# Performance work log

Measured on AMD Instinct MI355X. Metric: run time of the kernel, lower is better.

Reference implementation:

```python
import jax, jax.numpy as jnp
import numpy as np

N = 200000      # total nodes
NG = 100000     # masked (graph) nodes
NU = N - NG     # unconnected nodes
E = 3200000     # edges (index into graph nodes)
C = 1000000     # candidate pairs


def setup_inputs() -> dict:
    key = jax.random.key(0)
    ks = jax.random.split(key, 16)
    s = 0.1  # weight init scale
    x = jax.random.normal(ks[0], (N, 2), jnp.float32)
    mask = jnp.arange(N) < NG
    candidates = jnp.stack([
        jax.random.randint(ks[1], (C,), 0, NG),
        jax.random.randint(ks[2], (C,), 0, NU),
    ], axis=1).astype(jnp.int32)
    edges = jax.random.randint(ks[3], (2, E), 0, NG).astype(jnp.int32)
    return {
        "x": x, "mask": mask, "candidates": candidates, "edges": edges,
        # GraphConv(2,8): lin_rel on aggregated neighbors, lin_root on self, bias in rel
        "w1_rel": jax.random.normal(ks[4], (2, 8), jnp.float32) * s,
        "w1_root": jax.random.normal(ks[5], (2, 8), jnp.float32) * s,
        "b1": jnp.zeros((8,), jnp.float32),
        # GraphConv(8,16)
        "w2_rel": jax.random.normal(ks[6], (8, 16), jnp.float32) * s,
        "w2_root": jax.random.normal(ks[7], (8, 16), jnp.float32) * s,
        "b2": jnp.zeros((16,), jnp.float32),
        # fc_unconnected: Linear(2,16) (source's Linear(8,16) is inconsistent with 2-dim x)
        "wu": jax.random.normal(ks[8], (2, 16), jnp.float32) * s,
        "bu": jnp.zeros((16,), jnp.float32),
        # fc: Linear(32,64) -> ReLU -> Linear(64,1)
        "wa": jax.random.normal(ks[9], (32, 64), jnp.float32) * s,
        "ba": jnp.zeros((64,), jnp.float32),
        "wb": jax.random.normal(ks[10], (64, 1), jnp.float32) * s,
        "bb": jnp.zeros((1,), jnp.float32),
    }


def graph_conv(h, edges, w_rel, w_root, b, n):
    # PyG GraphConv with aggr='add': out_i = W_rel @ sum_{j->i} h_j + W_root @ h_i + b
    src, dst = edges[0], edges[1]
    agg = jax.ops.segment_sum(h[src], dst, num_segments=n)  # [n, d_in]
    return agg @ w_rel + h @ w_root + b


def reference(x, mask, candidates, edges, w1_rel, w1_root, b1,
              w2_rel, w2_root, b2, wu, bu, wa, ba, wb, bb):
    idx_g = jnp.nonzero(mask, size=NG)[0]      # graph node indices
    idx_u = jnp.nonzero(~mask, size=NU)[0]     # unconnected node indices
    x_unconnected = x[idx_u] @ wu + bu                         # [NU, 16]
    h = jax.nn.relu(graph_conv(x[idx_g], edges, w1_rel, w1_root, b1, NG))  # [NG, 8]
    h = jax.nn.relu(graph_conv(h, edges, w2_rel, w2_root, b2, NG))         # [NG, 16]
    ec = jnp.concatenate([h[candidates[:, 0]], x_unconnected[candidates[:, 1]]], axis=-1)  # [C, 32]
    hid = jax.nn.relu(ec @ wa + ba)            # [C, 64]
    return jnp.squeeze(hid @ wb + bb, -1)      # [C]
```

## Files before the change

kernel.cpp:

```cpp
#include <hip/hip_runtime.h>

#define N_TOT  200000
#define NG_    100000
#define NU_    100000
#define E_CNT  3200000
#define C_CNT  1000000

#define NBUCK  196
#define NBLK   256
#define CHUNK  12500

#define CBLK   250
#define CCHUNK 4000
#define CCH_E  3907

#define DCAP   17920


__global__ __launch_bounds__(1024) void phaseA_f(const int* __restrict__ dst,
                                                 const int* __restrict__ cand,
                                                 int* __restrict__ cnt_mat,
                                                 int* __restrict__ cnt2) {
    __shared__ int hcnt[NBUCK];
    int t = threadIdx.x;
    if (t < NBUCK) hcnt[t] = 0;
    __syncthreads();
    int beg = blockIdx.x * CHUNK, end = beg + CHUNK;
    for (int e = beg + t; e < end; e += 1024)
        atomicAdd(&hcnt[dst[e] >> 9], 1);
    __syncthreads();
    if (t < NBUCK) { cnt_mat[blockIdx.x * NBUCK + t] = hcnt[t]; hcnt[t] = 0; }
    __syncthreads();
    int cbeg = blockIdx.x * CCH_E;
    int cend = min(cbeg + CCH_E, C_CNT);
    for (int e = cbeg + t; e < cend; e += 1024)
        atomicAdd(&hcnt[cand[2 * e] >> 9], 1);
    __syncthreads();
    if (t < NBUCK) cnt2[blockIdx.x * NBUCK + t] = hcnt[t];
}

__global__ __launch_bounds__(256) void phaseB1_f(const int* __restrict__ cnt_mat,
                                                 const int* __restrict__ cnt2,
                                                 int* __restrict__ off_mat,
                                                 int* __restrict__ off2,
                                                 int* __restrict__ colsum,
                                                 int* __restrict__ csum2) {
    __shared__ int s[256];
    int t = threadIdx.x;
    int k = blockIdx.x % NBUCK;
    bool is_cand = blockIdx.x >= NBUCK;
    const int* cm = is_cand ? cnt2 : cnt_mat;
    int v = cm[t * NBUCK + k];
    s[t] = v;
    __syncthreads();
    for (int off = 1; off < 256; off <<= 1) {
        int u = (t >= off) ? s[t - off] : 0;
        __syncthreads();
        s[t] += u;
        __syncthreads();
    }
    int* om = is_cand ? off2 : off_mat;
    om[t * NBUCK + k] = s[t] - v;
    if (t == 255) (is_cand ? csum2 : colsum)[k] = s[255];
}

__global__ __launch_bounds__(256) void phaseB2_f(const int* __restrict__ colsum,
                                                 const int* __restrict__ csum2,
                                                 int* __restrict__ bbase,
                                                 int* __restrict__ bbase2,
                                                 const float* __restrict__ wu,
                                                 const float* __restrict__ bu,
                                                 const float* __restrict__ wa,
                                                 const float* __restrict__ ba,
                                                 float* __restrict__ wprep) {
    __shared__ int s[256];
    int t = threadIdx.x;
    int v = (t < NBUCK) ? colsum[t] : 0;
    s[t] = v;
    __syncthreads();
    for (int off = 1; off < 256; off <<= 1) {
        int u = (t >= off) ? s[t - off] : 0;
        __syncthreads();
        s[t] += u;
        __syncthreads();
    }
    if (t < NBUCK) bbase[t] = s[t] - v;
    if (t == NBUCK - 1) bbase[NBUCK] = s[t];
    __syncthreads();
    int v2 = (t < NBUCK) ? csum2[t] : 0;
    s[t] = v2;
    __syncthreads();
    for (int off = 1; off < 256; off <<= 1) {
        int u = (t >= off) ? s[t - off] : 0;
        __syncthreads();
        s[t] += u;
        __syncthreads();
    }
    if (t < NBUCK) bbase2[t] = s[t] - v2;
    if (t == NBUCK - 1) bbase2[NBUCK] = s[t];
    if (t < 64) {
        int j = t;
#pragma unroll
        for (int i = 0; i < 16; i++) wprep[j * 16 + i] = wa[i * 64 + j];
        float c0 = 0.f, c1 = 0.f, bc = ba[j];
#pragma unroll
        for (int k2 = 0; k2 < 16; k2++) {
            float w = wa[(16 + k2) * 64 + j];
            c0 += wu[k2] * w;
            c1 += wu[16 + k2] * w;
            bc += bu[k2] * w;
        }
        wprep[1024 + j] = c0;
        wprep[1088 + j] = c1;
        wprep[1152 + j] = bc;
    }
}

__global__ __launch_bounds__(1024) void phaseC_f(const int* __restrict__ src,
                                                 const int* __restrict__ dst,
                                                 const int* __restrict__ off_mat,
                                                 const int* __restrict__ bbase,
                                                 const int* __restrict__ cand,
                                                 const int* __restrict__ off2,
                                                 const int* __restrict__ bbase2,
                                                 int* __restrict__ pairs,
                                                 int2* __restrict__ sc) {
    __shared__ int loc[NBUCK];
    int t = threadIdx.x;
    if (t < NBUCK) loc[t] = bbase[t] + off_mat[blockIdx.x * NBUCK + t];
    __syncthreads();
    int beg = blockIdx.x * CHUNK, end = beg + CHUNK;
    for (int e = beg + t; e < end; e += 1024) {
        int d = dst[e], s = src[e];
        int k = d >> 9;
        int pos = atomicAdd(&loc[k], 1);
        pairs[pos] = (s << 9) | (d & 511);
    }
    __syncthreads();
    if (t < NBUCK) loc[t] = bbase2[t] + off2[blockIdx.x * NBUCK + t];
    __syncthreads();
    int cbeg = blockIdx.x * CCH_E;
    int cend = min(cbeg + CCH_E, C_CNT);
    for (int e = cbeg + t; e < cend; e += 1024) {
        int g = cand[2 * e], u = cand[2 * e + 1];
        int k = g >> 9;
        int pos = atomicAdd(&loc[k], 1);
        int w0 = g | (u << 17);
        int w1 = (int)(((unsigned)u >> 15) | ((unsigned)e << 2));
        sc[pos] = make_int2(w0, w1);
    }
}


__global__ __launch_bounds__(256) void phaseA(const int* __restrict__ dst,
                                              int* __restrict__ cnt_mat) {
    __shared__ int hcnt[NBUCK];
    int t = threadIdx.x;
    if (t < NBUCK) hcnt[t] = 0;
    __syncthreads();
    int beg = blockIdx.x * CHUNK, end = beg + CHUNK;
    for (int e = beg + t; e < end; e += 256)
        atomicAdd(&hcnt[dst[e] >> 9], 1);
    __syncthreads();
    if (t < NBUCK) cnt_mat[blockIdx.x * NBUCK + t] = hcnt[t];
}

__global__ __launch_bounds__(256) void phaseB1(const int* __restrict__ cnt_mat,
                                               int* __restrict__ off_mat,
                                               int* __restrict__ colsum) {
    __shared__ int s[256];
    int t = threadIdx.x;
    int k = blockIdx.x;
    int v = cnt_mat[t * NBUCK + k];
    s[t] = v;
    __syncthreads();
    for (int off = 1; off < 256; off <<= 1) {
        int u = (t >= off) ? s[t - off] : 0;
        __syncthreads();
        s[t] += u;
        __syncthreads();
    }
    off_mat[t * NBUCK + k] = s[t] - v;
    if (t == 255) colsum[k] = s[255];
}

__global__ __launch_bounds__(256) void phaseB2(const int* __restrict__ colsum,
                                               int* __restrict__ bbase) {
    __shared__ int s[256];
    int t = threadIdx.x;
    int v = (t < NBUCK) ? colsum[t] : 0;
    s[t] = v;
    __syncthreads();
    for (int off = 1; off < 256; off <<= 1) {
        int u = (t >= off) ? s[t - off] : 0;
        __syncthreads();
        s[t] += u;
        __syncthreads();
    }
    if (t < NBUCK) bbase[t] = s[t] - v;
    if (t == NBUCK - 1) bbase[NBUCK] = s[t];
}

__global__ __launch_bounds__(256) void phaseC(const int* __restrict__ src,
                                              const int* __restrict__ dst,
                                              const int* __restrict__ off_mat,
                                              const int* __restrict__ bbase,
                                              int* __restrict__ pairs) {
    __shared__ int loc[NBUCK];
    int t = threadIdx.x;
    if (t < NBUCK) loc[t] = bbase[t] + off_mat[blockIdx.x * NBUCK + t];
    __syncthreads();
    int beg = blockIdx.x * CHUNK, end = beg + CHUNK;
    for (int e = beg + t; e < end; e += 256) {
        int d = dst[e], s = src[e];
        int k = d >> 9;
        int pos = atomicAdd(&loc[k], 1);
        pairs[pos] = (s << 9) | (d & 511);
    }
}

__global__ void prep_kernel(const float* __restrict__ wu,
                            const float* __restrict__ bu,
                            const float* __restrict__ wa,
                            const float* __restrict__ ba,
                            float* __restrict__ wprep) {
    int j = threadIdx.x;
#pragma unroll
    for (int i = 0; i < 16; i++) wprep[j * 16 + i] = wa[i * 64 + j];
    float c0 = 0.f, c1 = 0.f, bc = ba[j];
#pragma unroll
    for (int k = 0; k < 16; k++) {
        float w = wa[(16 + k) * 64 + j];
        c0 += wu[k] * w;
        c1 += wu[16 + k] * w;
        bc += bu[k] * w;
    }
    wprep[1024 + j] = c0;
    wprep[1088 + j] = c1;
    wprep[1152 + j] = bc;
}

__global__ __launch_bounds__(256) void candA(const int* __restrict__ cand,
                                             int* __restrict__ cnt2) {
    __shared__ int hcnt[NBUCK];
    int t = threadIdx.x;
    if (t < NBUCK) hcnt[t] = 0;
    __syncthreads();
    int beg = blockIdx.x * CCHUNK, end = beg + CCHUNK;
    for (int e = beg + t; e < end; e += 256)
        atomicAdd(&hcnt[cand[2 * e] >> 9], 1);
    __syncthreads();
    if (t < NBUCK) cnt2[blockIdx.x * NBUCK + t] = hcnt[t];
}

__global__ __launch_bounds__(256) void candB1(const int* __restrict__ cnt2,
                                              int* __restrict__ off2,
                                              int* __restrict__ csum2) {
    __shared__ int s[256];
    int t = threadIdx.x;
    int k = blockIdx.x;
    int v = (t < CBLK) ? cnt2[t * NBUCK + k] : 0;
    s[t] = v;
    __syncthreads();
    for (int off = 1; off < 256; off <<= 1) {
        int u = (t >= off) ? s[t - off] : 0;
        __syncthreads();
        s[t] += u;
        __syncthreads();
    }
    if (t < CBLK) off2[t * NBUCK + k] = s[t] - v;
    if (t == 255) csum2[k] = s[255];
}

__global__ __launch_bounds__(256) void candB2(const int* __restrict__ csum2,
                                              int* __restrict__ bbase2) {
    __shared__ int s[256];
    int t = threadIdx.x;
    int v = (t < NBUCK) ? csum2[t] : 0;
    s[t] = v;
    __syncthreads();
    for (int off = 1; off < 256; off <<= 1) {
        int u = (t >= off) ? s[t - off] : 0;
        __syncthreads();
        s[t] += u;
        __syncthreads();
    }
    if (t < NBUCK) bbase2[t] = s[t] - v;
    if (t == NBUCK - 1) bbase2[NBUCK] = s[t];
}

__global__ __launch_bounds__(256) void candC(const int* __restrict__ cand,
                                             const int* __restrict__ off2,
                                             const int* __restrict__ bbase2,
                                             int2* __restrict__ sc) {
    __shared__ int loc[NBUCK];
    int t = threadIdx.x;
    if (t < NBUCK) loc[t] = bbase2[t] + off2[blockIdx.x * NBUCK + t];
    __syncthreads();
    int beg = blockIdx.x * CCHUNK, end = beg + CCHUNK;
    for (int e = beg + t; e < end; e += 256) {
        int g = cand[2 * e], u = cand[2 * e + 1];
        int k = g >> 9;
        int pos = atomicAdd(&loc[k], 1);
        int w0 = g | (u << 17);
        int w1 = (int)(((unsigned)u >> 15) | ((unsigned)e << 2));
        sc[pos] = make_int2(w0, w1);
    }
}


__global__ __launch_bounds__(1024) void phaseD(const int* __restrict__ bbase,
                                               const int* __restrict__ pairs,
                                               int* __restrict__ csr_src,
                                               int* __restrict__ node_off) {
    __shared__ int cnt[512], scn[512], base[512];
    __shared__ int lpairs[DCAP];
    int t = threadIdx.x, k = blockIdx.x;
    if (t < 512) cnt[t] = 0;
    __syncthreads();
    int beg = bbase[k], end = bbase[k + 1];
    int len = end - beg;
    for (int i = t; i < len; i += 1024) {
        int p = pairs[beg + i];
        if (i < DCAP) lpairs[i] = p;
        atomicAdd(&cnt[p & 511], 1);
    }
    __syncthreads();
    if (t < 512) scn[t] = cnt[t];
    __syncthreads();
    for (int off = 1; off < 512; off <<= 1) {
        int v = 0;
        if (t < 512 && t >= off) v = scn[t - off];
        __syncthreads();
        if (t < 512) scn[t] += v;
        __syncthreads();
    }
    if (t < 512) {
        int bse = beg + scn[t] - cnt[t];
        base[t] = bse;
        node_off[(k << 9) + t] = bse;
    }
    __syncthreads();
    for (int i = t; i < len; i += 1024) {
        int p = (i < DCAP) ? lpairs[i] : pairs[beg + i];
        int pos = atomicAdd(&base[p & 511], 1);
        csr_src[pos] = p >> 9;
    }
}

__global__ __launch_bounds__(256) void conv1_csr(const int* __restrict__ node_off,
                                                 const int* __restrict__ csr_src,
                                                 const float* __restrict__ x,
                                                 const float* __restrict__ w_rel,
                                                 const float* __restrict__ w_root,
                                                 const float* __restrict__ b,
                                                 float* __restrict__ h1) {
    int t = threadIdx.x;
    int n = blockIdx.x * 32 + (t >> 3);
    int l = t & 7;
    int beg = node_off[n], end = node_off[n + 1];
    float a0 = 0.f, a1 = 0.f, b0 = 0.f, b1v = 0.f;
    float c0 = 0.f, c1 = 0.f, d0 = 0.f, d1 = 0.f;
    int e = beg + l;
    for (; e + 24 < end; e += 32) {
        int s0 = csr_src[e];
        int s1 = csr_src[e + 8];
        int s2 = csr_src[e + 16];
        int s3 = csr_src[e + 24];
        float2 v0 = *(const float2*)(x + 2 * s0);
        float2 v1 = *(const float2*)(x + 2 * s1);
        float2 v2 = *(const float2*)(x + 2 * s2);
        float2 v3 = *(const float2*)(x + 2 * s3);
        a0 += v0.x; a1 += v0.y;
        b0 += v1.x; b1v += v1.y;
        c0 += v2.x; c1 += v2.y;
        d0 += v3.x; d1 += v3.y;
    }
    for (; e < end; e += 8) {
        int s0 = csr_src[e];
        float2 v0 = *(const float2*)(x + 2 * s0);
        a0 += v0.x; a1 += v0.y;
    }
    a0 += b0 + c0 + d0;
    a1 += b1v + c1 + d1;
#pragma unroll
    for (int d = 1; d < 8; d <<= 1) {
        a0 += __shfl_xor(a0, d, 64);
        a1 += __shfl_xor(a1, d, 64);
    }
    float2 xn = *(const float2*)(x + 2 * n);
    float v = a0 * w_rel[l] + a1 * w_rel[8 + l]
            + xn.x * w_root[l] + xn.y * w_root[8 + l] + b[l];
    h1[8 * n + l] = fmaxf(v, 0.f);
}

__global__ __launch_bounds__(256) void conv2_ag16(const int* __restrict__ node_off,
                                                  const int* __restrict__ csr_src,
                                                  const float* __restrict__ h1,
                                                  const float* __restrict__ w_rel,
                                                  const float* __restrict__ w_root,
                                                  const float* __restrict__ b,
                                                  const float* __restrict__ wa,
                                                  const float* __restrict__ wprep,
                                                  float* __restrict__ Ag) {
    __shared__ float sh[16][17];
    int t = threadIdx.x;
    int g = t >> 4, l = t & 15;
    int pr = l & 1, pe = l >> 1;
    int n = blockIdx.x * 16 + g;
    int beg = node_off[n], end = node_off[n + 1];
    float4 a4 = make_float4(0.f, 0.f, 0.f, 0.f);
    float4 b4 = make_float4(0.f, 0.f, 0.f, 0.f);
    float4 c4 = make_float4(0.f, 0.f, 0.f, 0.f);
    float4 d4 = make_float4(0.f, 0.f, 0.f, 0.f);
    int e = beg + pe;
    for (; e + 24 < end; e += 32) {
        int s0 = csr_src[e];
        int s1 = csr_src[e + 8];
        int s2 = csr_src[e + 16];
        int s3 = csr_src[e + 24];
        float4 v0 = *(const float4*)(h1 + 8 * s0 + 4 * pr);
        float4 v1 = *(const float4*)(h1 + 8 * s1 + 4 * pr);
        float4 v2 = *(const float4*)(h1 + 8 * s2 + 4 * pr);
        float4 v3 = *(const float4*)(h1 + 8 * s3 + 4 * pr);
        a4.x += v0.x; a4.y += v0.y; a4.z += v0.z; a4.w += v0.w;
        b4.x += v1.x; b4.y += v1.y; b4.z += v1.z; b4.w += v1.w;
        c4.x += v2.x; c4.y += v2.y; c4.z += v2.z; c4.w += v2.w;
        d4.x += v3.x; d4.y += v3.y; d4.z += v3.z; d4.w += v3.w;
    }
    for (; e < end; e += 8) {
        int s0 = csr_src[e];
        float4 v0 = *(const float4*)(h1 + 8 * s0 + 4 * pr);
        a4.x += v0.x; a4.y += v0.y; a4.z += v0.z; a4.w += v0.w;
    }
    a4.x += b4.x + c4.x + d4.x;
    a4.y += b4.y + c4.y + d4.y;
    a4.z += b4.z + c4.z + d4.z;
    a4.w += b4.w + c4.w + d4.w;
#pragma unroll
    for (int d = 2; d < 16; d <<= 1) {
        a4.x += __shfl_xor(a4.x, d);
        a4.y += __shfl_xor(a4.y, d);
        a4.z += __shfl_xor(a4.z, d);
        a4.w += __shfl_xor(a4.w, d);
    }
    float o0 = __shfl_xor(a4.x, 1), o1 = __shfl_xor(a4.y, 1);
    float o2 = __shfl_xor(a4.z, 1), o3 = __shfl_xor(a4.w, 1);
    float agg[8];
    if (pr == 0) {
        agg[0] = a4.x; agg[1] = a4.y; agg[2] = a4.z; agg[3] = a4.w;
        agg[4] = o0;   agg[5] = o1;   agg[6] = o2;   agg[7] = o3;
    } else {
        agg[0] = o0;   agg[1] = o1;   agg[2] = o2;   agg[3] = o3;
        agg[4] = a4.x; agg[5] = a4.y; agg[6] = a4.z; agg[7] = a4.w;
    }
    const float4* hp = (const float4*)(h1 + 8 * n);
    float4 t0 = hp[0], t1 = hp[1];
    float hn[8] = {t0.x, t0.y, t0.z, t0.w, t1.x, t1.y, t1.z, t1.w};
    {
        int c = l;
        float v = b[c];
#pragma unroll
        for (int j = 0; j < 8; j++)
            v += agg[j] * w_rel[j * 16 + c] + hn[j] * w_root[j * 16 + c];
        sh[g][c] = fmaxf(v, 0.f);
    }
    __syncthreads();
    float4 a = *(const float4*)(wprep + 1152 + 4 * l);
#pragma unroll
    for (int i = 0; i < 16; i++) {
        float hi = sh[g][i];
        float4 w = *(const float4*)(wa + i * 64 + 4 * l);
        a.x += hi * w.x; a.y += hi * w.y; a.z += hi * w.z; a.w += hi * w.w;
    }
    *(float4*)(Ag + 64 * n + 4 * l) = a;
}

__global__ __launch_bounds__(256) void conv2_csr(const int* __restrict__ node_off,
                                                 const int* __restrict__ csr_src,
                                                 const float* __restrict__ h1,
                                                 const float* __restrict__ w_rel,
                                                 const float* __restrict__ w_root,
                                                 const float* __restrict__ b,
                                                 float* __restrict__ h2) {
    int t = threadIdx.x;
    int n = blockIdx.x * 32 + (t >> 3);
    int l = t & 7;
    int beg = node_off[n], end = node_off[n + 1];
    float acc[8] = {0.f, 0.f, 0.f, 0.f, 0.f, 0.f, 0.f, 0.f};
    for (int e = beg + l; e < end; e += 8) {
        int s = csr_src[e];
        const float4* hp = (const float4*)(h1 + 8 * s);
        float4 v0 = hp[0], v1 = hp[1];
        acc[0] += v0.x; acc[1] += v0.y; acc[2] += v0.z; acc[3] += v0.w;
        acc[4] += v1.x; acc[5] += v1.y; acc[6] += v1.z; acc[7] += v1.w;
    }
#pragma unroll
    for (int d = 1; d < 8; d <<= 1)
#pragma unroll
        for (int j = 0; j < 8; j++)
            acc[j] += __shfl_xor(acc[j], d, 64);
    const float4* hp = (const float4*)(h1 + 8 * n);
    float4 t0 = hp[0], t1 = hp[1];
    float hn[8] = {t0.x, t0.y, t0.z, t0.w, t1.x, t1.y, t1.z, t1.w};
#pragma unroll
    for (int cc = 0; cc < 2; cc++) {
        int c = l + 8 * cc;
        float v = b[c];
#pragma unroll
        for (int j = 0; j < 8; j++)
            v += acc[j] * w_rel[j * 16 + c] + hn[j] * w_root[j * 16 + c];
        h2[16 * n + c] = fmaxf(v, 0.f);
    }
}

__global__ __launch_bounds__(256) void precompA(const float* __restrict__ h2,
                                                const float* __restrict__ wa,
                                                const float* __restrict__ wprep,
                                                float* __restrict__ Ag) {
    int g = blockIdx.x * 256 + threadIdx.x;
    if (g >= NG_) return;
    float h[16];
    const float4* hp = (const float4*)(h2 + 16 * g);
#pragma unroll
    for (int q = 0; q < 4; q++) {
        float4 v = hp[q];
        h[4*q] = v.x; h[4*q+1] = v.y; h[4*q+2] = v.z; h[4*q+3] = v.w;
    }
    float4* op = (float4*)(Ag + 64 * g);
#pragma unroll
    for (int q = 0; q < 16; q++) {
        float4 v;
        v.x = wprep[1152 + 4*q + 0];
        v.y = wprep[1152 + 4*q + 1];
        v.z = wprep[1152 + 4*q + 2];
        v.w = wprep[1152 + 4*q + 3];
#pragma unroll
        for (int i = 0; i < 16; i++) {
            float hi = h[i];
            v.x += hi * wa[i*64 + 4*q + 0];
            v.y += hi * wa[i*64 + 4*q + 1];
            v.z += hi * wa[i*64 + 4*q + 2];
            v.w += hi * wa[i*64 + 4*q + 3];
        }
        op[q] = v;
    }
}

__global__ __launch_bounds__(256) void final_mlp7(const int2* __restrict__ sc,
                                                  const float* __restrict__ Ag,
                                                  const float* __restrict__ x,
                                                  const float* __restrict__ wprep,
                                                  const float* __restrict__ wb,
                                                  const float* __restrict__ bb,
                                                  float* __restrict__ out) {
    int nwg = gridDim.x;
    int xcd = blockIdx.x & 7, pos = blockIdx.x >> 3;
    int q = nwg >> 3, r = nwg & 7;
    int wg = (xcd < r ? xcd * (q + 1) : r * (q + 1) + (xcd - r) * q) + pos;

    int t = threadIdx.x;
    int l = t & 7;
    int grp = t >> 3;
    float4 c0lo = *(const float4*)(wprep + 1024 + 4 * l);
    float4 c0hi = *(const float4*)(wprep + 1024 + 32 + 4 * l);
    float4 c1lo = *(const float4*)(wprep + 1088 + 4 * l);
    float4 c1hi = *(const float4*)(wprep + 1088 + 32 + 4 * l);
    float4 wblo = *(const float4*)(wb + 4 * l);
    float4 wbhi = *(const float4*)(wb + 32 + 4 * l);
    float bb0 = bb[0];

    int base = wg * 256;
#pragma unroll 2
    for (int it = 0; it < 8; ++it) {
        int c = base + it * 32 + grp;
        if (c < C_CNT) {
            int2 w = sc[c];
            unsigned w0 = (unsigned)w.x, w1 = (unsigned)w.y;
            int g   = (int)(w0 & 0x1FFFFu);
            int u   = (int)((w0 >> 17) | ((w1 & 3u) << 15));
            int idx = (int)(w1 >> 2);
            float2 xv = *(const float2*)(x + 2 * (NG_ + u));
            const float* rp = Ag + 64 * g;
            float4 alo = *(const float4*)(rp + 4 * l);
            float4 ahi = *(const float4*)(rp + 32 + 4 * l);
            float acc;
            {
                float v0 = alo.x + xv.x * c0lo.x + xv.y * c1lo.x;
                float v1 = alo.y + xv.x * c0lo.y + xv.y * c1lo.y;
                float v2 = alo.z + xv.x * c0lo.z + xv.y * c1lo.z;
                float v3 = alo.w + xv.x * c0lo.w + xv.y * c1lo.w;
                acc  = fmaxf(v0, 0.f) * wblo.x;
                acc += fmaxf(v1, 0.f) * wblo.y;
                acc += fmaxf(v2, 0.f) * wblo.z;
                acc += fmaxf(v3, 0.f) * wblo.w;
            }
            {
                float v0 = ahi.x + xv.x * c0hi.x + xv.y * c1hi.x;
                float v1 = ahi.y + xv.x * c0hi.y + xv.y * c1hi.y;
                float v2 = ahi.z + xv.x * c0hi.z + xv.y * c1hi.z;
                float v3 = ahi.w + xv.x * c0hi.w + xv.y * c1hi.w;
                acc += fmaxf(v0, 0.f) * wbhi.x;
                acc += fmaxf(v1, 0.f) * wbhi.y;
                acc += fmaxf(v2, 0.f) * wbhi.z;
                acc += fmaxf(v3, 0.f) * wbhi.w;
            }
            acc += __shfl_xor(acc, 1);
            acc += __shfl_xor(acc, 2);
            acc += __shfl_xor(acc, 4);
            if (l == 0) out[idx] = acc + bb0;
        }
    }
}


extern "C" void kernel_launch(void* const* d_in, const int* in_sizes, int n_in,
                              void* d_out, int out_size, void* d_ws, size_t ws_size,
                              hipStream_t stream) {
    const float* x      = (const float*)d_in[0];
    const int*   cand   = (const int*)d_in[2];
    const int*   edges  = (const int*)d_in[3];
    const float* w1_rel = (const float*)d_in[4];
    const float* w1_root= (const float*)d_in[5];
    const float* b1     = (const float*)d_in[6];
    const float* w2_rel = (const float*)d_in[7];
    const float* w2_root= (const float*)d_in[8];
    const float* b2     = (const float*)d_in[9];
    const float* wu     = (const float*)d_in[10];
    const float* bu     = (const float*)d_in[11];
    const float* wa     = (const float*)d_in[12];
    const float* ba     = (const float*)d_in[13];
    const float* wb     = (const float*)d_in[14];
    const float* bb     = (const float*)d_in[15];
    float* out = (float*)d_out;

    const int* src = edges;
    const int* dst = edges + E_CNT;

    int* ws_i = (int*)d_ws;
    int*   cnt_mat  = ws_i;
    int*   off_mat  = ws_i + 50176;
    int*   colsum   = ws_i + 100352;
    int*   bbase    = ws_i + 100608;
    int*   node_off = ws_i + 100864;
    float* wprep    = (float*)(ws_i + 201728);
    int*   pairs    = ws_i + 202944;
    int*   csr_src  = ws_i + 3402944;
    float* h1       = (float*)(ws_i + 6602944);
    float* h2       = (float*)(ws_i + 7402944);

    bool ext = ws_size >= (size_t)17503808 * sizeof(int);

    dim3 blk256(256);
    dim3 blk1024(1024);

    if (ext) {
        int*   cnt2   = ws_i + 9002944;
        int*   off2   = ws_i + 9053120;
        int*   csum2  = ws_i + 9103296;
        int*   bbase2 = ws_i + 9103552;
        int2*  sc     = (int2*)(ws_i + 9103808);
        float* Ag     = (float*)(ws_i + 11103808);

        phaseA_f <<<NBLK, blk1024, 0, stream>>>(dst, cand, cnt_mat, cnt2);
        phaseB1_f<<<2 * NBUCK, blk256, 0, stream>>>(cnt_mat, cnt2, off_mat, off2,
                                                    colsum, csum2);
        phaseB2_f<<<1, blk256, 0, stream>>>(colsum, csum2, bbase, bbase2,
                                            wu, bu, wa, ba, wprep);
        phaseC_f <<<NBLK, blk1024, 0, stream>>>(src, dst, off_mat, bbase,
                                                cand, off2, bbase2, pairs, sc);
        phaseD <<<NBUCK, blk1024, 0, stream>>>(bbase, pairs, csr_src, node_off);
        conv1_csr<<<3125, blk256, 0, stream>>>(node_off, csr_src, x, w1_rel, w1_root, b1, h1);
        conv2_ag16<<<6250, blk256, 0, stream>>>(node_off, csr_src, h1, w2_rel, w2_root, b2,
                                                wa, wprep, Ag);
        final_mlp7<<<(C_CNT + 255) / 256, blk256, 0, stream>>>(sc, Ag, x, wprep, wb, bb, out);
    } else {
        int*   cnt2   = ws_i;
        int*   off2   = ws_i + 50176;
        int*   csum2  = ws_i + 100352;
        int*   bbase2 = ws_i + 100608;
        int2*  sc     = (int2*)(ws_i + 6602944);
        float* Ag     = (float*)(ws_i + 202944);

        prep_kernel<<<1, 64, 0, stream>>>(wu, bu, wa, ba, wprep);
        phaseA <<<NBLK, blk256, 0, stream>>>(dst, cnt_mat);
        phaseB1<<<NBUCK, blk256, 0, stream>>>(cnt_mat, off_mat, colsum);
        phaseB2<<<1, blk256, 0, stream>>>(colsum, bbase);
        phaseC <<<NBLK, blk256, 0, stream>>>(src, dst, off_mat, bbase, pairs);
        phaseD <<<NBUCK, blk1024, 0, stream>>>(bbase, pairs, csr_src, node_off);
        conv1_csr<<<3125, blk256, 0, stream>>>(node_off, csr_src, x, w1_rel, w1_root, b1, h1);
        conv2_csr<<<3125, blk256, 0, stream>>>(node_off, csr_src, h1, w2_rel, w2_root, b2, h2);
        precompA<<<(NG_ + 255) / 256, blk256, 0, stream>>>(h2, wa, wprep, Ag);
        candA <<<CBLK, blk256, 0, stream>>>(cand, cnt2);
        candB1<<<NBUCK, blk256, 0, stream>>>(cnt2, off2, csum2);
        candB2<<<1, blk256, 0, stream>>>(csum2, bbase2);
        candC <<<CBLK, blk256, 0, stream>>>(cand, off2, bbase2, sc);
        final_mlp7<<<(C_CNT + 255) / 256, blk256, 0, stream>>>(sc, Ag, x, wprep, wb, bb, out);
    }
}
```

Before: 243.7 us.

## Compute per-node CSR offsets via global atomic counts instead of in-bucket histogram

```diff
diff --git a/kernel.cpp b/kernel.cpp
--- a/kernel.cpp
+++ b/kernel.cpp
@@ -17,17 +17,26 @@
 #define DCAP   17920
 
 
+__global__ __launch_bounds__(1024) void zeroN(int* __restrict__ node_cnt) {
+    int i = blockIdx.x * 1024 + threadIdx.x;
+    if (i < NG_) node_cnt[i] = 0;
+}
+
 __global__ __launch_bounds__(1024) void phaseA_f(const int* __restrict__ dst,
                                                  const int* __restrict__ cand,
                                                  int* __restrict__ cnt_mat,
-                                                 int* __restrict__ cnt2) {
+                                                 int* __restrict__ cnt2,
+                                                 int* __restrict__ node_cnt) {
     __shared__ int hcnt[NBUCK];
     int t = threadIdx.x;
     if (t < NBUCK) hcnt[t] = 0;
     __syncthreads();
     int beg = blockIdx.x * CHUNK, end = beg + CHUNK;
-    for (int e = beg + t; e < end; e += 1024)
-        atomicAdd(&hcnt[dst[e] >> 9], 1);
+    for (int e = beg + t; e < end; e += 1024) {
+        int d = dst[e];
+        atomicAdd(&hcnt[d >> 9], 1);
+        atomicAdd(&node_cnt[d], 1);
+    }
     __syncthreads();
     if (t < NBUCK) { cnt_mat[blockIdx.x * NBUCK + t] = hcnt[t]; hcnt[t] = 0; }
     __syncthreads();
@@ -116,6 +125,25 @@
     }
 }
 
+__global__ __launch_bounds__(512) void scanN(const int* __restrict__ node_cnt,
+                                             const int* __restrict__ bbase,
+                                             int* __restrict__ node_off) {
+    __shared__ int s[512];
+    int k = blockIdx.x, t = threadIdx.x;
+    int idx = (k << 9) + t;
+    int v = (idx < NG_) ? node_cnt[idx] : 0;
+    s[t] = v;
+    __syncthreads();
+    for (int off = 1; off < 512; off <<= 1) {
+        int u = (t >= off) ? s[t - off] : 0;
+        __syncthreads();
+        s[t] += u;
+        __syncthreads();
+    }
+    if (idx < NG_) node_off[idx] = bbase[k] + s[t] - v;
+    if (k == 0 && t == 0) node_off[NG_] = E_CNT;
+}
+
 __global__ __launch_bounds__(1024) void phaseC_f(const int* __restrict__ src,
                                                  const int* __restrict__ dst,
                                                  const int* __restrict__ off_mat,
@@ -151,6 +179,25 @@
     }
 }
 
+__global__ __launch_bounds__(1024) void phaseD2(const int* __restrict__ bbase,
+                                                const int* __restrict__ node_off,
+                                                const int* __restrict__ pairs,
+                                                int* __restrict__ csr_src) {
+    __shared__ int cur[512];
+    int t = threadIdx.x, k = blockIdx.x;
+    if (t < 512) {
+        int idx = (k << 9) + t;
+        cur[t] = (idx < NG_) ? node_off[idx] : 0;
+    }
+    __syncthreads();
+    int beg = bbase[k], end = bbase[k + 1];
+    for (int e = beg + t; e < end; e += 1024) {
+        int p = pairs[e];
+        int pos = atomicAdd(&cur[p & 511], 1);
+        csr_src[pos] = p >> 9;
+    }
+}
+
 
 __global__ __launch_bounds__(256) void phaseA(const int* __restrict__ dst,
                                               int* __restrict__ cnt_mat) {
@@ -308,7 +355,6 @@
     }
 }
 
-
 __global__ __launch_bounds__(1024) void phaseD(const int* __restrict__ bbase,
                                                const int* __restrict__ pairs,
                                                int* __restrict__ csr_src,
@@ -347,6 +393,7 @@
         csr_src[pos] = p >> 9;
     }
 }
+
 
 __global__ __launch_bounds__(256) void conv1_csr(const int* __restrict__ node_off,
                                                  const int* __restrict__ csr_src,
@@ -649,27 +696,31 @@
     float* h1       = (float*)(ws_i + 6602944);
     float* h2       = (float*)(ws_i + 7402944);
 
-    bool ext = ws_size >= (size_t)17503808 * sizeof(int);
+    bool ext = ws_size >= (size_t)17603808 * sizeof(int);
 
     dim3 blk256(256);
+    dim3 blk512(512);
     dim3 blk1024(1024);
 
     if (ext) {
-        int*   cnt2   = ws_i + 9002944;
-        int*   off2   = ws_i + 9053120;
-        int*   csum2  = ws_i + 9103296;
-        int*   bbase2 = ws_i + 9103552;
-        int2*  sc     = (int2*)(ws_i + 9103808);
-        float* Ag     = (float*)(ws_i + 11103808);
-
-        phaseA_f <<<NBLK, blk1024, 0, stream>>>(dst, cand, cnt_mat, cnt2);
+        int*   cnt2     = ws_i + 9002944;
+        int*   off2     = ws_i + 9053120;
+        int*   csum2    = ws_i + 9103296;
+        int*   bbase2   = ws_i + 9103552;
+        int2*  sc       = (int2*)(ws_i + 9103808);
+        float* Ag       = (float*)(ws_i + 11103808);
+        int*   node_cnt = ws_i + 17503808;
+
+        zeroN    <<<(NG_ + 1023) / 1024, blk1024, 0, stream>>>(node_cnt);
+        phaseA_f <<<NBLK, blk1024, 0, stream>>>(dst, cand, cnt_mat, cnt2, node_cnt);
         phaseB1_f<<<2 * NBUCK, blk256, 0, stream>>>(cnt_mat, cnt2, off_mat, off2,
                                                     colsum, csum2);
         phaseB2_f<<<1, blk256, 0, stream>>>(colsum, csum2, bbase, bbase2,
                                             wu, bu, wa, ba, wprep);
+        scanN    <<<NBUCK, blk512, 0, stream>>>(node_cnt, bbase, node_off);
         phaseC_f <<<NBLK, blk1024, 0, stream>>>(src, dst, off_mat, bbase,
                                                 cand, off2, bbase2, pairs, sc);
-        phaseD <<<NBUCK, blk1024, 0, stream>>>(bbase, pairs, csr_src, node_off);
+        phaseD2  <<<NBUCK, blk1024, 0, stream>>>(bbase, node_off, pairs, csr_src);
         conv1_csr<<<3125, blk256, 0, stream>>>(node_off, csr_src, x, w1_rel, w1_root, b1, h1);
         conv2_ag16<<<6250, blk256, 0, stream>>>(node_off, csr_src, h1, w2_rel, w2_root, b2,
                                                 wa, wprep, Ag);
```

New measurement: 380.9 us. +56.3%, slower.
